# Performance work log

Hardware: AMD Instinct MI355X
Metric: run time of the kernel (lower is better)

Reference implementation:

```python
import jax, jax.numpy as jnp
import numpy as np

TEMPERATURE = 0.1
EPS = 1e-12  # F.normalize default eps


def _l2norm(x):
    n = jnp.sqrt(jnp.sum(x * x, axis=-1, keepdims=True))
    return x / jnp.maximum(n, EPS)


def setup_inputs() -> dict:
    key = jax.random.key(0)
    k1, k2, k3 = jax.random.split(key, 3)
    G, NA, NO, D = 256, 256, 512, 128
    student_nodes = jax.random.normal(k1, (G * NA, D), dtype=jnp.float32)
    teacher_nodes = jax.random.normal(k2, (G * NO, D), dtype=jnp.float32)
    # local indices into each original graph's node block (as in t_nodes_all[kept_indices])
    kept_node_indices = jax.random.randint(k3, (G * NA,), 0, NO, dtype=jnp.int64)
    return {
        "student_nodes": student_nodes,
        "teacher_nodes": teacher_nodes,
        "kept_node_indices": kept_node_indices,
        "num_graphs": G,
        "n_aug": NA,
        "n_orig": NO,
    }


def reference(student_nodes, teacher_nodes, kept_node_indices, num_graphs, n_aug, n_orig):
    D = student_nodes.shape[-1]
    # ragged batch regularized: ptr boundaries -> fixed-size reshape
    s = _l2norm(student_nodes.reshape(num_graphs, n_aug, D))      # [G, Na, D]
    t = _l2norm(teacher_nodes.reshape(num_graphs, n_orig, D))     # [G, No, D]
    kept = kept_node_indices.reshape(num_graphs, n_aug)           # [G, Na]
    t_aligned = jnp.take_along_axis(t, kept[:, :, None], axis=1)  # [G, Na, D]
    scores = jnp.einsum("gid,gjd->gij", s, t_aligned) / TEMPERATURE  # [G, Na, Na]
    logp = jax.nn.log_softmax(scores, axis=-1)
    idx = jnp.arange(n_aug)
    # CE with labels = arange: -logp[g, i, i], mean over i per graph, then mean over graphs
    per_graph_ce = -jnp.mean(logp[:, idx, idx], axis=-1)          # [G]
    return jnp.mean(per_graph_ce)
```

## Files before the change

kernel.cpp:

```cpp
#include <hip/hip_runtime.h>
#include <hip/hip_bf16.h>

using f32x4  = __attribute__((ext_vector_type(4))) float;
using bf16x8 = __attribute__((ext_vector_type(8))) short;

constexpr int   G_NUM = 256;
constexpr int   NAUG  = 256;
constexpr int   NORIG = 512;
constexpr int   DIM   = 128;
constexpr float INV_T = 10.0f;

__device__ __forceinline__ short f32_to_bf16_bits(float x) {
    unsigned u = __float_as_uint(x);
    u += 0x7fffu + ((u >> 16) & 1u);
    return (short)(u >> 16);
}

__global__ __launch_bounds__(512, 1) void nlcl_main(
    const float* __restrict__ student,
    const float* __restrict__ teacher,
    const int*   __restrict__ kept,
    float*       __restrict__ graph_sums)
{
    __shared__ short t_lds[NAUG * DIM];

    const int g    = blockIdx.x;
    const int tid  = threadIdx.x;
    const int lane = tid & 63;
    const int wave = tid >> 6;

    const float* s_base = student + (size_t)g * NAUG * DIM;
    const float* t_base = teacher + (size_t)g * NORIG * DIM;
    const int*   k_base = kept + g * NAUG;

    const int ccol  = lane & 15;
    const int cquad = lane >> 4;

    bf16x8 afrag[2][4];
    #pragma unroll
    for (int rt = 0; rt < 2; ++rt) {
        const int row = wave * 32 + rt * 16 + ccol;
        const float* rp = s_base + row * DIM;
        float sf[4][8];
        #pragma unroll
        for (int kc = 0; kc < 4; ++kc) {
            const int d0 = kc * 32 + cquad * 8;
            const float4 a = *reinterpret_cast<const float4*>(rp + d0);
            const float4 b = *reinterpret_cast<const float4*>(rp + d0 + 4);
            sf[kc][0] = a.x; sf[kc][1] = a.y; sf[kc][2] = a.z; sf[kc][3] = a.w;
            sf[kc][4] = b.x; sf[kc][5] = b.y; sf[kc][6] = b.z; sf[kc][7] = b.w;
        }
        float ss = 0.f;
        #pragma unroll
        for (int kc = 0; kc < 4; ++kc)
            #pragma unroll
            for (int e = 0; e < 8; ++e) ss += sf[kc][e] * sf[kc][e];
        ss += __shfl_xor(ss, 16);
        ss += __shfl_xor(ss, 32);
        const float scale = rsqrtf(fmaxf(ss, 1e-24f));
        #pragma unroll
        for (int kc = 0; kc < 4; ++kc)
            #pragma unroll
            for (int e = 0; e < 8; ++e)
                afrag[rt][kc][e] = f32_to_bf16_bits(sf[kc][e] * scale);
    }

    {
        const int hw = tid >> 5;
        const int hl = tid & 31;
        char* tl = reinterpret_cast<char*>(t_lds);
        #pragma unroll 4
        for (int it = 0; it < 16; ++it) {
            const int j   = it * 16 + hw;
            const int src = k_base[j];
            const float* rp = t_base + (size_t)src * DIM;
            const float4 v = *reinterpret_cast<const float4*>(rp + hl * 4);
            float ss = v.x * v.x + v.y * v.y + v.z * v.z + v.w * v.w;
            ss += __shfl_xor(ss, 1);
            ss += __shfl_xor(ss, 2);
            ss += __shfl_xor(ss, 4);
            ss += __shfl_xor(ss, 8);
            ss += __shfl_xor(ss, 16);
            const float scale = rsqrtf(fmaxf(ss, 1e-24f));
            short4 o;
            o.x = f32_to_bf16_bits(v.x * scale);
            o.y = f32_to_bf16_bits(v.y * scale);
            o.z = f32_to_bf16_bits(v.z * scale);
            o.w = f32_to_bf16_bits(v.w * scale);
            const int byte = j * 256 + ((hl * 8) ^ ((j & 7) << 4));
            *reinterpret_cast<short4*>(tl + byte) = o;
        }
    }
    __syncthreads();

    float sumexp[2][4] = {{0.f, 0.f, 0.f, 0.f}, {0.f, 0.f, 0.f, 0.f}};
    float diagsum = 0.f;
    const char* tl = reinterpret_cast<const char*>(t_lds);

    for (int ct = 0; ct < 16; ++ct) {
        f32x4 acc0 = {0.f, 0.f, 0.f, 0.f};
        f32x4 acc1 = {0.f, 0.f, 0.f, 0.f};
        const int j = ct * 16 + ccol;
        #pragma unroll
        for (int kc = 0; kc < 4; ++kc) {
            const int byte = j * 256 + (((kc * 64) + (cquad * 16)) ^ ((j & 7) << 4));
            const bf16x8 b = *reinterpret_cast<const bf16x8*>(tl + byte);
            acc0 = __builtin_amdgcn_mfma_f32_16x16x32_bf16(afrag[0][kc], b, acc0, 0, 0, 0);
            acc1 = __builtin_amdgcn_mfma_f32_16x16x32_bf16(afrag[1][kc], b, acc1, 0, 0, 0);
        }
        const int col = j;
        #pragma unroll
        for (int reg = 0; reg < 4; ++reg) {
            const int row0 = wave * 32 + cquad * 4 + reg;
            const int row1 = row0 + 16;
            const float l0 = acc0[reg] * INV_T;
            const float l1 = acc1[reg] * INV_T;
            sumexp[0][reg] += __expf(l0);
            sumexp[1][reg] += __expf(l1);
            if (col == row0) diagsum += l0;
            if (col == row1) diagsum += l1;
        }
    }

    float ce = 0.f;
    #pragma unroll
    for (int rt = 0; rt < 2; ++rt) {
        #pragma unroll
        for (int reg = 0; reg < 4; ++reg) {
            float s = sumexp[rt][reg];
            s += __shfl_xor(s, 1);
            s += __shfl_xor(s, 2);
            s += __shfl_xor(s, 4);
            s += __shfl_xor(s, 8);
            if (ccol == 0) ce += __logf(s);
        }
    }
    ce -= diagsum;
    ce += __shfl_xor(ce, 1);
    ce += __shfl_xor(ce, 2);
    ce += __shfl_xor(ce, 4);
    ce += __shfl_xor(ce, 8);
    ce += __shfl_xor(ce, 16);
    ce += __shfl_xor(ce, 32);

    __syncthreads();
    float* red = reinterpret_cast<float*>(t_lds);
    if (lane == 0) red[wave] = ce;
    __syncthreads();
    if (tid == 0) {
        float t = 0.f;
        #pragma unroll
        for (int w = 0; w < 8; ++w) t += red[w];
        graph_sums[g] = t;
    }
}

__global__ void nlcl_reduce(const float* __restrict__ graph_sums,
                            float* __restrict__ out)
{
    __shared__ float r[4];
    const int tid = threadIdx.x;
    float v = graph_sums[tid];
    v += __shfl_xor(v, 1);
    v += __shfl_xor(v, 2);
    v += __shfl_xor(v, 4);
    v += __shfl_xor(v, 8);
    v += __shfl_xor(v, 16);
    v += __shfl_xor(v, 32);
    if ((tid & 63) == 0) r[tid >> 6] = v;
    __syncthreads();
    if (tid == 0)
        out[0] = (r[0] + r[1] + r[2] + r[3]) * (1.0f / ((float)G_NUM * (float)NAUG));
}

extern "C" void kernel_launch(void* const* d_in, const int* in_sizes, int n_in,
                              void* d_out, int out_size, void* d_ws, size_t ws_size,
                              hipStream_t stream) {
    (void)in_sizes; (void)n_in; (void)out_size; (void)ws_size;
    const float* student = (const float*)d_in[0];
    const float* teacher = (const float*)d_in[1];
    const int*   kept    = (const int*)d_in[2];
    float* gs  = (float*)d_ws;
    float* out = (float*)d_out;

    nlcl_main<<<G_NUM, 512, 0, stream>>>(student, teacher, kept, gs);
    nlcl_reduce<<<1, 256, 0, stream>>>(gs, out);
}
```

Baseline: 24.72 us.

## Split each graph across two blocks by row halves with XCD-aware block mapping

Launches 512 blocks instead of 256, with each block handling 128 student rows of one graph. Both blocks of a graph redundantly gather and normalize the full 256-row teacher tile into LDS. Block IDs are remapped so consecutive logical blocks spread across the 8 XCDs. All kept indices are prefetched into registers before the gather loop, which is now fully unrolled, and launch bounds allow more resident blocks. The aim is better CU occupancy and latency hiding, at the cost of doubling teacher gather traffic and normalization work.

```diff
diff --git a/kernel.cpp b/kernel.cpp
--- a/kernel.cpp
+++ b/kernel.cpp
@@ -16,18 +16,23 @@
     return (short)(u >> 16);
 }
 
-__global__ __launch_bounds__(512, 1) void nlcl_main(
+__global__ __launch_bounds__(512, 4) void nlcl_main(
     const float* __restrict__ student,
     const float* __restrict__ teacher,
     const int*   __restrict__ kept,
-    float*       __restrict__ graph_sums)
+    float*       __restrict__ block_sums)
 {
     __shared__ short t_lds[NAUG * DIM];
 
-    const int g    = blockIdx.x;
+    const int bid = blockIdx.x;
+    const int logical = (bid & 7) * 64 + (bid >> 3);
+    const int g    = logical >> 1;
+    const int half = logical & 1;
+
     const int tid  = threadIdx.x;
     const int lane = tid & 63;
     const int wave = tid >> 6;
+    const int rbase = half * 128;
 
     const float* s_base = student + (size_t)g * NAUG * DIM;
     const float* t_base = teacher + (size_t)g * NORIG * DIM;
@@ -36,10 +41,15 @@
     const int ccol  = lane & 15;
     const int cquad = lane >> 4;
 
-    bf16x8 afrag[2][4];
+    const int hw = tid >> 5;
+    const int hl = tid & 31;
+    int idxv[16];
     #pragma unroll
-    for (int rt = 0; rt < 2; ++rt) {
-        const int row = wave * 32 + rt * 16 + ccol;
+    for (int it = 0; it < 16; ++it) idxv[it] = k_base[it * 16 + hw];
+
+    bf16x8 afrag[4];
+    {
+        const int row = rbase + wave * 16 + ccol;
         const float* rp = s_base + row * DIM;
         float sf[4][8];
         #pragma unroll
@@ -62,18 +72,15 @@
         for (int kc = 0; kc < 4; ++kc)
             #pragma unroll
             for (int e = 0; e < 8; ++e)
-                afrag[rt][kc][e] = f32_to_bf16_bits(sf[kc][e] * scale);
+                afrag[kc][e] = f32_to_bf16_bits(sf[kc][e] * scale);
     }
 
     {
-        const int hw = tid >> 5;
-        const int hl = tid & 31;
         char* tl = reinterpret_cast<char*>(t_lds);
-        #pragma unroll 4
+        #pragma unroll
         for (int it = 0; it < 16; ++it) {
             const int j   = it * 16 + hw;
-            const int src = k_base[j];
-            const float* rp = t_base + (size_t)src * DIM;
+            const float* rp = t_base + (size_t)idxv[it] * DIM;
             const float4 v = *reinterpret_cast<const float4*>(rp + hl * 4);
             float ss = v.x * v.x + v.y * v.y + v.z * v.z + v.w * v.w;
             ss += __shfl_xor(ss, 1);
@@ -93,47 +100,37 @@
     }
     __syncthreads();
 
-    float sumexp[2][4] = {{0.f, 0.f, 0.f, 0.f}, {0.f, 0.f, 0.f, 0.f}};
+    float sumexp[4] = {0.f, 0.f, 0.f, 0.f};
     float diagsum = 0.f;
     const char* tl = reinterpret_cast<const char*>(t_lds);
 
     for (int ct = 0; ct < 16; ++ct) {
-        f32x4 acc0 = {0.f, 0.f, 0.f, 0.f};
-        f32x4 acc1 = {0.f, 0.f, 0.f, 0.f};
+        f32x4 acc = {0.f, 0.f, 0.f, 0.f};
         const int j = ct * 16 + ccol;
         #pragma unroll
         for (int kc = 0; kc < 4; ++kc) {
             const int byte = j * 256 + (((kc * 64) + (cquad * 16)) ^ ((j & 7) << 4));
             const bf16x8 b = *reinterpret_cast<const bf16x8*>(tl + byte);
-            acc0 = __builtin_amdgcn_mfma_f32_16x16x32_bf16(afrag[0][kc], b, acc0, 0, 0, 0);
-            acc1 = __builtin_amdgcn_mfma_f32_16x16x32_bf16(afrag[1][kc], b, acc1, 0, 0, 0);
+            acc = __builtin_amdgcn_mfma_f32_16x16x32_bf16(afrag[kc], b, acc, 0, 0, 0);
         }
-        const int col = j;
         #pragma unroll
         for (int reg = 0; reg < 4; ++reg) {
-            const int row0 = wave * 32 + cquad * 4 + reg;
-            const int row1 = row0 + 16;
-            const float l0 = acc0[reg] * INV_T;
-            const float l1 = acc1[reg] * INV_T;
-            sumexp[0][reg] += __expf(l0);
-            sumexp[1][reg] += __expf(l1);
-            if (col == row0) diagsum += l0;
-            if (col == row1) diagsum += l1;
+            const int row = rbase + wave * 16 + cquad * 4 + reg;
+            const float l = acc[reg] * INV_T;
+            sumexp[reg] += __expf(l);
+            if (j == row) diagsum += l;
         }
     }
 
     float ce = 0.f;
     #pragma unroll
-    for (int rt = 0; rt < 2; ++rt) {
-        #pragma unroll
-        for (int reg = 0; reg < 4; ++reg) {
-            float s = sumexp[rt][reg];
-            s += __shfl_xor(s, 1);
-            s += __shfl_xor(s, 2);
-            s += __shfl_xor(s, 4);
-            s += __shfl_xor(s, 8);
-            if (ccol == 0) ce += __logf(s);
-        }
+    for (int reg = 0; reg < 4; ++reg) {
+        float s = sumexp[reg];
+        s += __shfl_xor(s, 1);
+        s += __shfl_xor(s, 2);
+        s += __shfl_xor(s, 4);
+        s += __shfl_xor(s, 8);
+        if (ccol == 0) ce += __logf(s);
     }
     ce -= diagsum;
     ce += __shfl_xor(ce, 1);
@@ -151,16 +148,16 @@
         float t = 0.f;
         #pragma unroll
         for (int w = 0; w < 8; ++w) t += red[w];
-        graph_sums[g] = t;
+        block_sums[bid] = t;
     }
 }
 
-__global__ void nlcl_reduce(const float* __restrict__ graph_sums,
+__global__ void nlcl_reduce(const float* __restrict__ block_sums,
                             float* __restrict__ out)
 {
-    __shared__ float r[4];
+    __shared__ float r[8];
     const int tid = threadIdx.x;
-    float v = graph_sums[tid];
+    float v = block_sums[tid];
     v += __shfl_xor(v, 1);
     v += __shfl_xor(v, 2);
     v += __shfl_xor(v, 4);
@@ -169,8 +166,12 @@
     v += __shfl_xor(v, 32);
     if ((tid & 63) == 0) r[tid >> 6] = v;
     __syncthreads();
-    if (tid == 0)
-        out[0] = (r[0] + r[1] + r[2] + r[3]) * (1.0f / ((float)G_NUM * (float)NAUG));
+    if (tid == 0) {
+        float t = 0.f;
+        #pragma unroll
+        for (int w = 0; w < 8; ++w) t += r[w];
+        out[0] = t * (1.0f / ((float)G_NUM * (float)NAUG));
+    }
 }
 
 extern "C" void kernel_launch(void* const* d_in, const int* in_sizes, int n_in,
@@ -180,9 +181,9 @@
     const float* student = (const float*)d_in[0];
     const float* teacher = (const float*)d_in[1];
     const int*   kept    = (const int*)d_in[2];
-    float* gs  = (float*)d_ws;
+    float* bs  = (float*)d_ws;
     float* out = (float*)d_out;
 
-    nlcl_main<<<G_NUM, 512, 0, stream>>>(student, teacher, kept, gs);
-    nlcl_reduce<<<1, 256, 0, stream>>>(gs, out);
+    nlcl_main<<<512, 512, 0, stream>>>(student, teacher, kept, bs);
+    nlcl_reduce<<<1, 512, 0, stream>>>(bs, out);
 }
```

Result: no change. 24.45 us (-1.1%).

## Stage teacher rows via async global-to-LDS loads and overlap with MFMA halves

Applied to the files above, without the earlier changes.

The teacher gather now uses global_load_lds into a padded staging buffer, issued in two halves. The second half's loads are in flight while MFMA and softmax run on the first 128 columns. Student loads and kept-index loads are hoisted up front so their latency overlaps. The kernel adds more LDS and syncthreads, and launch bounds now request two blocks per CU, though with 256 blocks on 256 CUs that probably changes little.

```diff
diff --git a/kernel.cpp b/kernel.cpp
--- a/kernel.cpp
+++ b/kernel.cpp
@@ -9,6 +9,10 @@
 constexpr int   NORIG = 512;
 constexpr int   DIM   = 128;
 constexpr float INV_T = 10.0f;
+constexpr int   NBLK  = 256;
+
+constexpr int PAIR_PITCH = 1040;
+constexpr int STAGE_BYTES = 64 * PAIR_PITCH;
 
 __device__ __forceinline__ short f32_to_bf16_bits(float x) {
     unsigned u = __float_as_uint(x);
@@ -16,13 +20,15 @@
     return (short)(u >> 16);
 }
 
-__global__ __launch_bounds__(512, 1) void nlcl_main(
+__global__ __launch_bounds__(512, 2) void nlcl_main(
     const float* __restrict__ student,
     const float* __restrict__ teacher,
     const int*   __restrict__ kept,
-    float*       __restrict__ graph_sums)
+    float*       __restrict__ block_sums)
 {
-    __shared__ short t_lds[NAUG * DIM];
+    __shared__ __align__(16) char  stage[STAGE_BYTES];
+    __shared__ __align__(16) short tile[NAUG * DIM];
+    __shared__ float red[8];
 
     const int g    = blockIdx.x;
     const int tid  = threadIdx.x;
@@ -36,79 +42,114 @@
     const int ccol  = lane & 15;
     const int cquad = lane >> 4;
 
+    int srcv[16];
+    #pragma unroll
+    for (int t = 0; t < 16; ++t) {
+        const int pair = (t >> 3) * 64 + wave * 8 + (t & 7);
+        srcv[t] = k_base[pair * 2 + (lane >> 5)];
+    }
+
+    float4 sv[16];
+    #pragma unroll
+    for (int rt = 0; rt < 2; ++rt) {
+        const float* rp = s_base + (wave * 32 + rt * 16 + ccol) * DIM;
+        #pragma unroll
+        for (int kc = 0; kc < 4; ++kc) {
+            sv[rt * 8 + kc * 2]     = *reinterpret_cast<const float4*>(rp + kc * 32 + cquad * 8);
+            sv[rt * 8 + kc * 2 + 1] = *reinterpret_cast<const float4*>(rp + kc * 32 + cquad * 8 + 4);
+        }
+    }
+
+    #pragma unroll
+    for (int i = 0; i < 8; ++i) {
+        const float* src = t_base + (size_t)srcv[i] * DIM + (lane & 31) * 4;
+        char* dst = stage + (wave * 8 + i) * PAIR_PITCH;
+        __builtin_amdgcn_global_load_lds(
+            (const __attribute__((address_space(1))) void*)src,
+            (__attribute__((address_space(3))) void*)dst, 16, 0, 0);
+    }
+
     bf16x8 afrag[2][4];
     #pragma unroll
     for (int rt = 0; rt < 2; ++rt) {
-        const int row = wave * 32 + rt * 16 + ccol;
-        const float* rp = s_base + row * DIM;
-        float sf[4][8];
-        #pragma unroll
-        for (int kc = 0; kc < 4; ++kc) {
-            const int d0 = kc * 32 + cquad * 8;
-            const float4 a = *reinterpret_cast<const float4*>(rp + d0);
-            const float4 b = *reinterpret_cast<const float4*>(rp + d0 + 4);
-            sf[kc][0] = a.x; sf[kc][1] = a.y; sf[kc][2] = a.z; sf[kc][3] = a.w;
-            sf[kc][4] = b.x; sf[kc][5] = b.y; sf[kc][6] = b.z; sf[kc][7] = b.w;
-        }
         float ss = 0.f;
         #pragma unroll
-        for (int kc = 0; kc < 4; ++kc)
-            #pragma unroll
-            for (int e = 0; e < 8; ++e) ss += sf[kc][e] * sf[kc][e];
+        for (int q = 0; q < 8; ++q) {
+            const float4 v = sv[rt * 8 + q];
+            ss += v.x * v.x + v.y * v.y + v.z * v.z + v.w * v.w;
+        }
         ss += __shfl_xor(ss, 16);
         ss += __shfl_xor(ss, 32);
         const float scale = rsqrtf(fmaxf(ss, 1e-24f));
         #pragma unroll
-        for (int kc = 0; kc < 4; ++kc)
+        for (int kc = 0; kc < 4; ++kc) {
+            const float4 a = sv[rt * 8 + kc * 2], b = sv[rt * 8 + kc * 2 + 1];
+            afrag[rt][kc][0] = f32_to_bf16_bits(a.x * scale);
+            afrag[rt][kc][1] = f32_to_bf16_bits(a.y * scale);
+            afrag[rt][kc][2] = f32_to_bf16_bits(a.z * scale);
+            afrag[rt][kc][3] = f32_to_bf16_bits(a.w * scale);
+            afrag[rt][kc][4] = f32_to_bf16_bits(b.x * scale);
+            afrag[rt][kc][5] = f32_to_bf16_bits(b.y * scale);
+            afrag[rt][kc][6] = f32_to_bf16_bits(b.z * scale);
+            afrag[rt][kc][7] = f32_to_bf16_bits(b.w * scale);
+        }
+    }
+
+    __syncthreads();
+
+    char* tb = reinterpret_cast<char*>(tile);
+    {
+        const int row_l = tid >> 2;
+        const int sub   = tid & 3;
+        const int j     = row_l;
+        const char* sp = stage + (row_l >> 1) * PAIR_PITCH + (row_l & 1) * 512 + sub * 128;
+        float vals[32]; float ss = 0.f;
+        #pragma unroll
+        for (int it = 0; it < 8; ++it) {
+            const float4 v = *reinterpret_cast<const float4*>(sp + it * 16);
+            vals[it * 4] = v.x; vals[it * 4 + 1] = v.y;
+            vals[it * 4 + 2] = v.z; vals[it * 4 + 3] = v.w;
+            ss += v.x * v.x + v.y * v.y + v.z * v.z + v.w * v.w;
+        }
+        ss += __shfl_xor(ss, 1);
+        ss += __shfl_xor(ss, 2);
+        const float scale = rsqrtf(fmaxf(ss, 1e-24f));
+        #pragma unroll
+        for (int p = 0; p < 4; ++p) {
+            bf16x8 o;
             #pragma unroll
-            for (int e = 0; e < 8; ++e)
-                afrag[rt][kc][e] = f32_to_bf16_bits(sf[kc][e] * scale);
-    }
-
-    {
-        const int hw = tid >> 5;
-        const int hl = tid & 31;
-        char* tl = reinterpret_cast<char*>(t_lds);
-        #pragma unroll 4
-        for (int it = 0; it < 16; ++it) {
-            const int j   = it * 16 + hw;
-            const int src = k_base[j];
-            const float* rp = t_base + (size_t)src * DIM;
-            const float4 v = *reinterpret_cast<const float4*>(rp + hl * 4);
-            float ss = v.x * v.x + v.y * v.y + v.z * v.z + v.w * v.w;
-            ss += __shfl_xor(ss, 1);
-            ss += __shfl_xor(ss, 2);
-            ss += __shfl_xor(ss, 4);
-            ss += __shfl_xor(ss, 8);
-            ss += __shfl_xor(ss, 16);
-            const float scale = rsqrtf(fmaxf(ss, 1e-24f));
-            short4 o;
-            o.x = f32_to_bf16_bits(v.x * scale);
-            o.y = f32_to_bf16_bits(v.y * scale);
-            o.z = f32_to_bf16_bits(v.z * scale);
-            o.w = f32_to_bf16_bits(v.w * scale);
-            const int byte = j * 256 + ((hl * 8) ^ ((j & 7) << 4));
-            *reinterpret_cast<short4*>(tl + byte) = o;
-        }
-    }
-    __syncthreads();
-
-    float sumexp[2][4] = {{0.f, 0.f, 0.f, 0.f}, {0.f, 0.f, 0.f, 0.f}};
+            for (int e = 0; e < 8; ++e) o[e] = f32_to_bf16_bits(vals[p * 8 + e] * scale);
+            const int byte = j * 256 + ((sub * 64 + p * 16) ^ ((j & 7) << 4));
+            *reinterpret_cast<bf16x8*>(tb + byte) = o;
+        }
+    }
+    __syncthreads();
+
+    #pragma unroll
+    for (int i = 0; i < 8; ++i) {
+        const float* src = t_base + (size_t)srcv[8 + i] * DIM + (lane & 31) * 4;
+        char* dst = stage + (wave * 8 + i) * PAIR_PITCH;
+        __builtin_amdgcn_global_load_lds(
+            (const __attribute__((address_space(1))) void*)src,
+            (__attribute__((address_space(3))) void*)dst, 16, 0, 0);
+    }
+
+    float sumexp[2][4] = {{0.f,0.f,0.f,0.f},{0.f,0.f,0.f,0.f}};
     float diagsum = 0.f;
-    const char* tl = reinterpret_cast<const char*>(t_lds);
-
-    for (int ct = 0; ct < 16; ++ct) {
-        f32x4 acc0 = {0.f, 0.f, 0.f, 0.f};
-        f32x4 acc1 = {0.f, 0.f, 0.f, 0.f};
+    const char* tlc = reinterpret_cast<const char*>(tile);
+
+    #pragma unroll 2
+    for (int ct = 0; ct < 8; ++ct) {
+        f32x4 acc0 = {0.f,0.f,0.f,0.f};
+        f32x4 acc1 = {0.f,0.f,0.f,0.f};
         const int j = ct * 16 + ccol;
         #pragma unroll
         for (int kc = 0; kc < 4; ++kc) {
             const int byte = j * 256 + (((kc * 64) + (cquad * 16)) ^ ((j & 7) << 4));
-            const bf16x8 b = *reinterpret_cast<const bf16x8*>(tl + byte);
+            const bf16x8 b = *reinterpret_cast<const bf16x8*>(tlc + byte);
             acc0 = __builtin_amdgcn_mfma_f32_16x16x32_bf16(afrag[0][kc], b, acc0, 0, 0, 0);
             acc1 = __builtin_amdgcn_mfma_f32_16x16x32_bf16(afrag[1][kc], b, acc1, 0, 0, 0);
         }
-        const int col = j;
         #pragma unroll
         for (int reg = 0; reg < 4; ++reg) {
             const int row0 = wave * 32 + cquad * 4 + reg;
@@ -117,8 +158,61 @@
             const float l1 = acc1[reg] * INV_T;
             sumexp[0][reg] += __expf(l0);
             sumexp[1][reg] += __expf(l1);
-            if (col == row0) diagsum += l0;
-            if (col == row1) diagsum += l1;
+            if (j == row0) diagsum += l0;
+            if (j == row1) diagsum += l1;
+        }
+    }
+    __syncthreads();
+
+    {
+        const int row_l = tid >> 2;
+        const int sub   = tid & 3;
+        const int j     = 128 + row_l;
+        const char* sp = stage + (row_l >> 1) * PAIR_PITCH + (row_l & 1) * 512 + sub * 128;
+        float vals[32]; float ss = 0.f;
+        #pragma unroll
+        for (int it = 0; it < 8; ++it) {
+            const float4 v = *reinterpret_cast<const float4*>(sp + it * 16);
+            vals[it * 4] = v.x; vals[it * 4 + 1] = v.y;
+            vals[it * 4 + 2] = v.z; vals[it * 4 + 3] = v.w;
+            ss += v.x * v.x + v.y * v.y + v.z * v.z + v.w * v.w;
+        }
+        ss += __shfl_xor(ss, 1);
+        ss += __shfl_xor(ss, 2);
+        const float scale = rsqrtf(fmaxf(ss, 1e-24f));
+        #pragma unroll
+        for (int p = 0; p < 4; ++p) {
+            bf16x8 o;
+            #pragma unroll
+            for (int e = 0; e < 8; ++e) o[e] = f32_to_bf16_bits(vals[p * 8 + e] * scale);
+            const int byte = j * 256 + ((sub * 64 + p * 16) ^ ((j & 7) << 4));
+            *reinterpret_cast<bf16x8*>(tb + byte) = o;
+        }
+    }
+    __syncthreads();
+
+    #pragma unroll 2
+    for (int ct = 8; ct < 16; ++ct) {
+        f32x4 acc0 = {0.f,0.f,0.f,0.f};
+        f32x4 acc1 = {0.f,0.f,0.f,0.f};
+        const int j = ct * 16 + ccol;
+        #pragma unroll
+        for (int kc = 0; kc < 4; ++kc) {
+            const int byte = j * 256 + (((kc * 64) + (cquad * 16)) ^ ((j & 7) << 4));
+            const bf16x8 b = *reinterpret_cast<const bf16x8*>(tlc + byte);
+            acc0 = __builtin_amdgcn_mfma_f32_16x16x32_bf16(afrag[0][kc], b, acc0, 0, 0, 0);
+            acc1 = __builtin_amdgcn_mfma_f32_16x16x32_bf16(afrag[1][kc], b, acc1, 0, 0, 0);
+        }
+        #pragma unroll
+        for (int reg = 0; reg < 4; ++reg) {
+            const int row0 = wave * 32 + cquad * 4 + reg;
+            const int row1 = row0 + 16;
+            const float l0 = acc0[reg] * INV_T;
+            const float l1 = acc1[reg] * INV_T;
+            sumexp[0][reg] += __expf(l0);
+            sumexp[1][reg] += __expf(l1);
+            if (j == row0) diagsum += l0;
+            if (j == row1) diagsum += l1;
         }
     }
 
@@ -143,24 +237,22 @@
     ce += __shfl_xor(ce, 16);
     ce += __shfl_xor(ce, 32);
 
-    __syncthreads();
-    float* red = reinterpret_cast<float*>(t_lds);
     if (lane == 0) red[wave] = ce;
     __syncthreads();
     if (tid == 0) {
         float t = 0.f;
         #pragma unroll
         for (int w = 0; w < 8; ++w) t += red[w];
-        graph_sums[g] = t;
-    }
-}
-
-__global__ void nlcl_reduce(const float* __restrict__ graph_sums,
+        block_sums[g] = t;
+    }
+}
+
+__global__ void nlcl_reduce(const float* __restrict__ block_sums,
                             float* __restrict__ out)
 {
     __shared__ float r[4];
     const int tid = threadIdx.x;
-    float v = graph_sums[tid];
+    float v = block_sums[tid];
     v += __shfl_xor(v, 1);
     v += __shfl_xor(v, 2);
     v += __shfl_xor(v, 4);
@@ -180,9 +272,9 @@
     const float* student = (const float*)d_in[0];
     const float* teacher = (const float*)d_in[1];
     const int*   kept    = (const int*)d_in[2];
-    float* gs  = (float*)d_ws;
+    float* bs  = (float*)d_ws;
     float* out = (float*)d_out;
 
-    nlcl_main<<<G_NUM, 512, 0, stream>>>(student, teacher, kept, gs);
-    nlcl_reduce<<<1, 256, 0, stream>>>(gs, out);
-}
+    nlcl_main<<<NBLK, 512, 0, stream>>>(student, teacher, kept, bs);
+    nlcl_reduce<<<1, 256, 0, stream>>>(bs, out);
+}
```

Result: faster. 23.16 us (-6.3%).
